# Kernel tuning notes

Measured on AMD Instinct MI355X. Metric: run time of the kernel, lower is better.

Reference implementation:

```python
import jax, jax.numpy as jnp
import numpy as np

EPS = 1e-5
C = 256
K = 3
K2 = K * K


def conv2d(x, w, b=None, groups=1):
    out = jax.lax.conv_general_dilated(
        x, w, (1, 1), 'VALID',
        dimension_numbers=('NCHW', 'OIHW', 'NCHW'),
        feature_group_count=groups)
    if b is not None:
        out = out + b[None, :, None, None]
    return out


def _bilinear_one(img, py, px):
    # img: [C,H,W]; py,px: [K2,ho,wo] float sampling coords (zero outside)
    _, H, W = img.shape
    y0 = jnp.floor(py)
    x0 = jnp.floor(px)
    dy = py - y0
    dx = px - x0
    y0i = y0.astype(jnp.int32)
    x0i = x0.astype(jnp.int32)

    def gather(yi, xi):
        valid = ((yi >= 0) & (yi < H) & (xi >= 0) & (xi < W)).astype(img.dtype)
        yc = jnp.clip(yi, 0, H - 1)
        xc = jnp.clip(xi, 0, W - 1)
        return img[:, yc, xc] * valid[None]  # [C,K2,ho,wo]

    w00 = (1 - dy) * (1 - dx)
    w01 = (1 - dy) * dx
    w10 = dy * (1 - dx)
    w11 = dy * dx
    return (gather(y0i, x0i) * w00[None] + gather(y0i, x0i + 1) * w01[None]
            + gather(y0i + 1, x0i) * w10[None] + gather(y0i + 1, x0i + 1) * w11[None])


def deform_conv(x, off_w, off_b, w, b):
    # ModulatedDeformConvPack: 3x3, stride=1, pad=0, dil=1, deformable_groups=1
    B, Cin, H, W = x.shape
    ho, wo = H - 2, W - 2
    om = conv2d(x, off_w, off_b)  # [B, 3*K2, ho, wo]
    o1, o2, m = om[:, :K2], om[:, K2:2 * K2], om[:, 2 * K2:]
    offset = jnp.concatenate([o1, o2], axis=1)  # [B, 2*K2, ho, wo]
    off_y = offset[:, 0::2]  # kernel reads y at channel 2k
    off_x = offset[:, 1::2]  # and x at channel 2k+1
    mask = jax.nn.sigmoid(m)  # [B,K2,ho,wo]
    ky, kx = jnp.meshgrid(jnp.arange(K), jnp.arange(K), indexing='ij')
    base_y = (ky.reshape(K2, 1, 1) + jnp.arange(ho).reshape(1, ho, 1)).astype(x.dtype)
    base_x = (kx.reshape(K2, 1, 1) + jnp.arange(wo).reshape(1, 1, wo)).astype(x.dtype)
    py = base_y[None] + off_y
    px = base_x[None] + off_x
    samples = jax.vmap(_bilinear_one)(x, py, px)  # [B,C,K2,ho,wo]
    samples = samples * mask[:, None]
    out = jnp.einsum('bckhw,ock->bohw', samples, w.reshape(w.shape[0], Cin, K2))
    return out + b[None, :, None, None]


def bn(x, g, b_, m, v):
    scale = g / jnp.sqrt(v + EPS)
    return (x - m[None, :, None, None]) * scale[None, :, None, None] + b_[None, :, None, None]


def xcorr(inst, exam):
    # batch-as-groups depthwise cross-correlation
    B = exam.shape[0]
    w = exam.reshape(B * C, 1, 18, 18)
    x = inst.reshape(1, B * C, 30, 30)
    out = jax.lax.conv_general_dilated(
        x, w, (1, 1), 'VALID',
        dimension_numbers=('NCHW', 'OIHW', 'NCHW'),
        feature_group_count=B * C)
    return out.reshape(B, C, 13, 13)


def _forward(examplar, instance, off_w, off_b, dcn_w, dcn_b,
             bn1_g, bn1_b, bn1_m, bn1_v,
             fus_w, fus_b, bn2_g, bn2_b, bn2_m, bn2_v,
             cls_w, cls_b, box_w, box_b):
    def head(x, i):  # deform conv + BN (eval)
        y = deform_conv(x, off_w[i], off_b[i], dcn_w[i], dcn_b[i])
        return bn(y, bn1_g[i], bn1_b[i], bn1_m[i], bn1_v[i])

    exam_cls = head(examplar, 0)
    inst_cls = head(instance, 1)
    exam_reg = head(examplar, 2)
    inst_reg = head(instance, 3)

    xc_cls = xcorr(inst_cls, exam_cls)
    xc_reg = xcorr(inst_reg, exam_reg)

    def fuse(x, i):  # 1x1 conv + BN + ReLU
        y = jnp.einsum('bchw,oc->bohw', x, fus_w[i]) + fus_b[i][None, :, None, None]
        return jax.nn.relu(bn(y, bn2_g[i], bn2_b[i], bn2_m[i], bn2_v[i]))

    f_cls = fuse(xc_cls, 0)
    f_reg = fuse(xc_reg, 1)

    cls_pred = jnp.einsum('bchw,oc->bohw', f_cls, cls_w) + cls_b[None, :, None, None]
    box_pred = jnp.einsum('bchw,oc->bohw', f_reg, box_w) + box_b[None, :, None, None]
    return cls_pred, box_pred


def setup_inputs() -> dict:
    key = jax.random.key(0)
    ks = jax.random.split(key, 24)
    B = 16
    d = {
        'examplar': jax.random.normal(ks[0], (B, C, 20, 20), jnp.float32),
        'instance': jax.random.normal(ks[1], (B, C, 32, 32), jnp.float32),
        # 4 deform heads: 0=exam_cls, 1=inst_cls, 2=exam_reg, 3=inst_reg
        'off_w': jax.random.normal(ks[2], (4, 3 * K2, C, K, K), jnp.float32) * 0.01,
        'off_b': jax.random.normal(ks[3], (4, 3 * K2), jnp.float32) * 0.01,
        'dcn_w': jax.random.normal(ks[4], (4, C, C, K, K), jnp.float32) * 0.05,
        'dcn_b': jax.random.normal(ks[5], (4, C), jnp.float32) * 0.05,
        'bn1_g': jax.random.uniform(ks[6], (4, C), jnp.float32) + 0.5,
        'bn1_b': jax.random.normal(ks[7], (4, C), jnp.float32) * 0.1,
        'bn1_m': jax.random.normal(ks[8], (4, C), jnp.float32) * 0.1,
        'bn1_v': jax.random.uniform(ks[9], (4, C), jnp.float32) + 0.5,
        # 2 fusion modules: 0=cls, 1=reg
        'fus_w': jax.random.normal(ks[10], (2, C, C), jnp.float32) * 0.05,
        'fus_b': jax.random.normal(ks[11], (2, C), jnp.float32) * 0.05,
        'bn2_g': jax.random.uniform(ks[12], (2, C), jnp.float32) + 0.5,
        'bn2_b': jax.random.normal(ks[13], (2, C), jnp.float32) * 0.1,
        'bn2_m': jax.random.normal(ks[14], (2, C), jnp.float32) * 0.1,
        'bn2_v': jax.random.uniform(ks[15], (2, C), jnp.float32) + 0.5,
        'cls_w': jax.random.normal(ks[16], (4, C), jnp.float32) * 0.05,
        'cls_b': jax.random.normal(ks[17], (4,), jnp.float32) * 0.05,
        'box_w': jax.random.normal(ks[18], (16, C), jnp.float32) * 0.05,
        'box_b': jax.random.normal(ks[19], (16,), jnp.float32) * 0.05,
    }
    return d


def reference(examplar, instance, off_w, off_b, dcn_w, dcn_b,
              bn1_g, bn1_b, bn1_m, bn1_v,
              fus_w, fus_b, bn2_g, bn2_b, bn2_m, bn2_v,
              cls_w, cls_b, box_w, box_b):
    return _forward(examplar, instance, off_w, off_b, dcn_w, dcn_b,
                    bn1_g, bn1_b, bn1_m, bn1_v,
                    fus_w, fus_b, bn2_g, bn2_b, bn2_m, bn2_v,
                    cls_w, cls_b, box_w, box_b)
```

## Files before the change

### kernel.cpp

```cpp
#include <hip/hip_runtime.h>
#include <math.h>

#define EPSBN 1e-5f

typedef _Float16 f16x8 __attribute__((ext_vector_type(8)));
typedef _Float16 f16x2 __attribute__((ext_vector_type(2)));
typedef float    f32x4 __attribute__((ext_vector_type(4)));

__device__ __forceinline__ f16x8 splat8(float v) {
  _Float16 h = (_Float16)v;
  return (f16x8){h, h, h, h, h, h, h, h};
}

static constexpr size_t XF_EX = 0;
static constexpr size_t XF_IN = 819200;
static constexpr size_t WPK   = 2916352;
static constexpr size_t OWPK  = 4096000;
static constexpr size_t FWT   = 4243456;
static constexpr size_t OM0   = 4374528;
static constexpr size_t OM1   = 4514496;
static constexpr size_t OM2   = 4903296;
static constexpr size_t OM3   = 5043264;
static constexpr size_t HOUT0 = 5432064;
static constexpr size_t HOUT1 = 6759168;
static constexpr size_t HOUT2 = 10445568;
static constexpr size_t HOUT3 = 11772672;
static constexpr size_t XCB   = 15459072;

__global__ __launch_bounds__(256) void k_transpose(const float* __restrict__ in,
                                                   _Float16* __restrict__ out,
                                                   int H, int W) {
  int y = blockIdx.x, b = blockIdx.y;
  __shared__ float tile[32][257];
  int t = threadIdx.x;
  int x = t & 31, cb = t >> 5;
  for (int c0 = 0; c0 < 256; c0 += 8) {
    int c = c0 + cb;
    if (x < W) tile[x][c] = in[(((size_t)b * 256 + c) * H + y) * W + x];
  }
  __syncthreads();
  for (int x2 = 0; x2 < W; ++x2)
    out[((((size_t)b * H + y) * W + x2) << 8) + t] = (_Float16)tile[x2][t];
}

__global__ __launch_bounds__(256) void k_wpack(const float* __restrict__ w,
                                               _Float16* __restrict__ wp) {
  int idx = blockIdx.x * 256 + threadIdx.x;
  if (idx >= 4 * 9 * 8 * 16 * 64 * 8) return;
  int e  = idx & 7;
  int l  = (idx >> 3) & 63;
  int ot = (idx >> 9) & 15;
  int cs = (idx >> 13) & 7;
  int ht = idx >> 16;
  int tap = ht % 9, h = ht / 9;
  int o = ot * 16 + (l & 15);
  int c = cs * 32 + 8 * (l >> 4) + e;
  wp[idx] = (_Float16)w[((size_t)((h * 256 + o) * 256 + c)) * 9 + tap];
}

__global__ __launch_bounds__(256) void k_owpack(const float* __restrict__ w,
                                                _Float16* __restrict__ wp) {
  int idx = blockIdx.x * 256 + threadIdx.x;
  if (idx >= 4 * 9 * 8 * 2 * 64 * 8) return;
  int e  = idx & 7;
  int l  = (idx >> 3) & 63;
  int ot = (idx >> 9) & 1;
  int cs = (idx >> 10) & 7;
  int ht = idx >> 13;
  int tap = ht % 9, h = ht / 9;
  int o = ot * 16 + (l & 15);
  int c = cs * 32 + 8 * (l >> 4) + e;
  wp[idx] = (o < 27) ? (_Float16)w[((size_t)((h * 27 + o) * 256 + c)) * 9 + tap]
                     : (_Float16)0.f;
}

__global__ __launch_bounds__(256) void k_fwt(const float* __restrict__ w,
                                             float* __restrict__ wt) {
  int idx = blockIdx.x * 256 + threadIdx.x;
  int o = idx & 255, c = (idx >> 8) & 255, i = idx >> 16;
  wt[idx] = w[(i << 16) + (o << 8) + c];
}

__global__ __launch_bounds__(256) void k_offdirect(const _Float16* __restrict__ xh_ex,
                                                   const _Float16* __restrict__ xh_in,
                                                   const _Float16* __restrict__ owpk,
                                                   const float* __restrict__ off_b,
                                                   float* __restrict__ ws) {
  const int h = blockIdx.z, b = blockIdx.y;
  const int HH[4] = {20, 32, 20, 32};
  const size_t OMO[4] = {OM0, OM1, OM2, OM3};
  const int H = HH[h], W = H, ho = H - 2, wo = W - 2, P = ho * wo;
  const int nblk = (P + 63) >> 6;
  if (blockIdx.x >= nblk) return;
  const int p0 = blockIdx.x << 6;
  const _Float16* xh = ((h & 1) ? xh_in : xh_ex) + (((size_t)b * H * W) << 8);

  const int t = threadIdx.x, lane = t & 63, wave = t >> 6;
  int p = min(p0 + wave * 16 + (lane & 15), P - 1);
  int i = p / wo, j = p - i * wo;
  const _Float16* xrow = xh + ((i * W + j) << 8) + 8 * (lane >> 4);

  f32x4 acc0 = {0.f, 0.f, 0.f, 0.f}, acc1 = {0.f, 0.f, 0.f, 0.f};
  for (int tap = 0; tap < 9; ++tap) {
    int ky = tap / 3, kx = tap - ky * 3;
    const _Float16* xt = xrow + ((ky * W + kx) << 8);
    const _Float16* ab0 = owpk + ((size_t)(h * 72 + tap * 8) * 2) * 512 + lane * 8;
    #pragma unroll
    for (int cs = 0; cs < 8; ++cs) {
      f16x8 bf = *(const f16x8*)(xt + cs * 32);
      f16x8 a0 = *(const f16x8*)(ab0 + (size_t)cs * 1024);
      f16x8 a1 = *(const f16x8*)(ab0 + (size_t)cs * 1024 + 512);
      acc0 = __builtin_amdgcn_mfma_f32_16x16x32_f16(a0, bf, acc0, 0, 0, 0);
      acc1 = __builtin_amdgcn_mfma_f32_16x16x32_f16(a1, bf, acc1, 0, 0, 0);
    }
  }
  float* om = ws + OMO[h] + (size_t)b * 27 * P;
  p = p0 + wave * 16 + (lane & 15);
  if (p < P) {
    #pragma unroll
    for (int r = 0; r < 4; ++r) {
      int o = 4 * (lane >> 4) + r;
      if (o < 27) om[o * P + p] = acc0[r] + off_b[h * 27 + o];
      int o2 = o + 16;
      if (o2 < 27) om[o2 * P + p] = acc1[r] + off_b[h * 27 + o2];
    }
  }
}

__global__ __launch_bounds__(256) void k_dgemm(const _Float16* __restrict__ xh_ex,
                                               const _Float16* __restrict__ xh_in,
                                               const _Float16* __restrict__ wpk,
                                               float* __restrict__ ws,
                                               const float* __restrict__ dcn_b,
                                               const float* __restrict__ g1,
                                               const float* __restrict__ b1,
                                               const float* __restrict__ m1,
                                               const float* __restrict__ v1) {
  const int h = blockIdx.z;
  const int HH4[4] = {20, 32, 20, 32};
  const size_t OMO[4] = {OM0, OM1, OM2, OM3};
  const size_t HOO[4] = {HOUT0, HOUT1, HOUT2, HOUT3};
  const int H = HH4[h], W = H, ho = H - 2, wo = W - 2, P = ho * wo;
  const int nblk = (P + 63) >> 6;
  if (blockIdx.x >= nblk) return;
  const int b = blockIdx.y;
  const int p0 = blockIdx.x << 6;
  const _Float16* xh = (h & 1) ? xh_in : xh_ex;
  const float* om = ws + OMO[h] + (size_t)b * 27 * P;
  float* outp = ws + HOO[h] + (size_t)b * 256 * P;

  __shared__ float4 swt4[576];
  __shared__ int4   sad4[576];
  __shared__ __align__(16) _Float16 S[64 * 256];

  const int t = threadIdx.x, lane = t & 63, wave = t >> 6;

  for (int e = t; e < 576; e += 256) {
    int pl = e / 9, k = e - pl * 9;
    float w4[4] = {0.f, 0.f, 0.f, 0.f};
    int a4[4] = {0, 0, 0, 0};
    int p = p0 + pl;
    if (p < P) {
      int i = p / wo, j = p - i * wo;
      float oy = om[(2 * k) * P + p];
      float ox = om[(2 * k + 1) * P + p];
      float mm = om[(18 + k) * P + p];
      float msk = 1.f / (1.f + __expf(-mm));
      int ky = k / 3, kx = k - ky * 3;
      float py = (float)(ky + i) + oy;
      float px = (float)(kx + j) + ox;
      float fy = floorf(py), fx = floorf(px);
      int y0 = (int)fy, x0 = (int)fx;
      float dy = py - fy, dx = px - fx;
      #pragma unroll
      for (int q = 0; q < 4; ++q) {
        int yy = y0 + (q >> 1), xx = x0 + (q & 1);
        bool vld = (yy >= 0) && (yy < H) && (xx < W) && (xx >= 0);
        int yc = min(max(yy, 0), H - 1), xc = min(max(xx, 0), W - 1);
        float wq = ((q >> 1) ? dy : 1.f - dy) * ((q & 1) ? dx : 1.f - dx);
        w4[q] = vld ? wq * msk : 0.f;
        a4[q] = ((blockIdx.y * H + yc) * W + xc) << 8;
      }
    }
    swt4[e] = make_float4(w4[0], w4[1], w4[2], w4[3]);
    sad4[e] = make_int4(a4[0], a4[1], a4[2], a4[3]);
  }

  f32x4 acc[4][4];
  #pragma unroll
  for (int a = 0; a < 4; ++a)
    #pragma unroll
    for (int n = 0; n < 4; ++n) acc[a][n] = (f32x4){0.f, 0.f, 0.f, 0.f};

  __syncthreads();

  const int o8 = t & 31;
  for (int tap = 0; tap < 9; ++tap) {
    #pragma unroll
    for (int it = 0; it < 8; ++it) {
      int pl = it * 8 + (t >> 5);
      float4 w4 = swt4[pl * 9 + tap];
      int4   a4 = sad4[pl * 9 + tap];
      const _Float16* xb = xh + o8 * 8;
      f16x8 x0 = *(const f16x8*)(xb + a4.x);
      f16x8 x1 = *(const f16x8*)(xb + a4.y);
      f16x8 x2 = *(const f16x8*)(xb + a4.z);
      f16x8 x3 = *(const f16x8*)(xb + a4.w);
      f16x8 s = x0 * splat8(w4.x) + x1 * splat8(w4.y) + x2 * splat8(w4.z) + x3 * splat8(w4.w);
      *(f16x8*)((char*)S + pl * 512 + ((o8 * 16) ^ ((pl & 7) << 4))) = s;
    }
    __syncthreads();
    #pragma unroll
    for (int cs = 0; cs < 8; ++cs) {
      int ksg = tap * 8 + cs;
      const _Float16* ab = wpk + ((size_t)(h * 72 + ksg) * 16 + wave * 4) * 512 + lane * 8;
      f16x8 A0 = *(const f16x8*)(ab);
      f16x8 A1 = *(const f16x8*)(ab + 512);
      f16x8 A2 = *(const f16x8*)(ab + 1024);
      f16x8 A3 = *(const f16x8*)(ab + 1536);
      f16x8 B[4];
      #pragma unroll
      for (int n = 0; n < 4; ++n) {
        int prow = n * 16 + (lane & 15);
        B[n] = *(const f16x8*)((char*)S + prow * 512 +
                               ((cs * 64 + ((lane >> 4) << 4)) ^ ((prow & 7) << 4)));
      }
      #pragma unroll
      for (int n = 0; n < 4; ++n) {
        acc[0][n] = __builtin_amdgcn_mfma_f32_16x16x32_f16(A0, B[n], acc[0][n], 0, 0, 0);
        acc[1][n] = __builtin_amdgcn_mfma_f32_16x16x32_f16(A1, B[n], acc[1][n], 0, 0, 0);
        acc[2][n] = __builtin_amdgcn_mfma_f32_16x16x32_f16(A2, B[n], acc[2][n], 0, 0, 0);
        acc[3][n] = __builtin_amdgcn_mfma_f32_16x16x32_f16(A3, B[n], acc[3][n], 0, 0, 0);
      }
    }
    __syncthreads();
  }

  #pragma unroll
  for (int a = 0; a < 4; ++a) {
    int obase = (wave * 4 + a) * 16 + 4 * (lane >> 4);
    #pragma unroll
    for (int r = 0; r < 4; ++r) {
      int o = obase + r;
      float al = g1[h * 256 + o] * rsqrtf(v1[h * 256 + o] + EPSBN);
      float be = (dcn_b[h * 256 + o] - m1[h * 256 + o]) * al + b1[h * 256 + o];
      #pragma unroll
      for (int n = 0; n < 4; ++n) {
        int p = p0 + n * 16 + (lane & 15);
        if (p < P) outp[(size_t)o * P + p] = fmaf(acc[a][n][r], al, be);
      }
    }
  }
}

__global__ __launch_bounds__(256) void k_xcorr3(float* __restrict__ ws) {
  const int br = blockIdx.y;
  const int bc0 = blockIdx.x << 4;
  const float* exg = ws + (br ? HOUT2 : HOUT0) + (size_t)bc0 * 324;
  const float* ing = ws + (br ? HOUT3 : HOUT1) + (size_t)bc0 * 900;
  __shared__ __align__(16) _Float16 exl[16 * 324];
  __shared__ __align__(16) _Float16 inl[16 * 960];
  const int t = threadIdx.x;
  for (int idx = t; idx < 16 * 324; idx += 256)
    exl[idx] = (_Float16)exg[idx];
  for (int idx = t; idx < 16 * 960; idx += 256) {
    int c = idx & 31;
    int rr = idx >> 5;
    inl[idx] = (c < 30) ? (_Float16)ing[rr * 30 + c] : (_Float16)0.f;
  }
  __syncthreads();
  const int lane = t & 63, wave = t >> 6;
  const int sub = lane / 13;
  const int i = lane - sub * 13;
  const bool active = sub < 4;
  const int bcl = wave * 4 + (active ? sub : 0);
  float acc[13];
  #pragma unroll
  for (int j = 0; j < 13; ++j) acc[j] = 0.f;
  const _Float16* inb = inl + bcl * 960;
  const _Float16* exb = exl + bcl * 324;
  for (int u = 0; u < 18; ++u) {
    float a[30];
    const _Float16* rp = inb + (i + u) * 32;
    #pragma unroll
    for (int x = 0; x < 15; ++x) {
      f16x2 pr = *(const f16x2*)(rp + 2 * x);
      a[2 * x] = (float)pr[0]; a[2 * x + 1] = (float)pr[1];
    }
    float e[18];
    const _Float16* ep = exb + u * 18;
    #pragma unroll
    for (int x = 0; x < 9; ++x) {
      f16x2 pr = *(const f16x2*)(ep + 2 * x);
      e[2 * x] = (float)pr[0]; e[2 * x + 1] = (float)pr[1];
    }
    #pragma unroll
    for (int v = 0; v < 18; ++v)
      #pragma unroll
      for (int j = 0; j < 13; ++j)
        acc[j] = fmaf(a[v + j], e[v], acc[j]);
  }
  if (active) {
    float* o = ws + XCB + ((size_t)(br * 4096 + bc0 + bcl)) * 169 + i * 13;
    #pragma unroll
    for (int j = 0; j < 13; ++j) o[j] = acc[j];
  }
}

__global__ __launch_bounds__(256) void k_fuse2(float* __restrict__ ws,
                                               const float* __restrict__ fus_b,
                                               const float* __restrict__ g2,
                                               const float* __restrict__ b2,
                                               const float* __restrict__ m2,
                                               const float* __restrict__ v2,
                                               const float* __restrict__ cls_w,
                                               const float* __restrict__ cls_b,
                                               const float* __restrict__ box_w,
                                               const float* __restrict__ box_b,
                                               float* __restrict__ out) {
  const int ij0 = blockIdx.x * 13;
  const int b = blockIdx.y;
  const int br = blockIdx.z;
  const int n_out = br ? 16 : 4;
  const float* ow = br ? box_w : cls_w;
  const float* ob = br ? box_b : cls_b;
  float* outp = out + (br ? (size_t)10816 : 0);

  __shared__ float xv[256 * 13];
  __shared__ float fv[13 * 257];
  const int t = threadIdx.x;
  const float* src = ws + XCB + ((size_t)br * 4096 + b * 256) * 169;
  for (int idx = t; idx < 256 * 13; idx += 256) {
    int c = idx / 13, j = idx - c * 13;
    xv[idx] = src[(size_t)c * 169 + ij0 + j];
  }
  __syncthreads();

  const float* fwt = ws + FWT + ((size_t)br << 16) + t;
  float acc[13];
  #pragma unroll
  for (int j = 0; j < 13; ++j) acc[j] = 0.f;
  for (int c = 0; c < 256; ++c) {
    float wv = fwt[c << 8];
    #pragma unroll
    for (int j = 0; j < 13; ++j)
      acc[j] = fmaf(wv, xv[c * 13 + j], acc[j]);
  }
  float s2 = g2[br * 256 + t] * rsqrtf(v2[br * 256 + t] + EPSBN);
  float fb = fus_b[br * 256 + t], mm = m2[br * 256 + t], bb = b2[br * 256 + t];
  #pragma unroll
  for (int j = 0; j < 13; ++j)
    fv[j * 257 + t] = fmaxf((acc[j] + fb - mm) * s2 + bb, 0.f);
  __syncthreads();

  const int g = t >> 4, l16 = t & 15;
  for (int wi = g; wi < 13 * n_out; wi += 16) {
    int j = wi / n_out, po = wi - j * n_out;
    float part = 0.f;
    #pragma unroll
    for (int q = 0; q < 16; ++q)
      part = fmaf(ow[(po << 8) + l16 + (q << 4)], fv[j * 257 + l16 + (q << 4)], part);
    #pragma unroll
    for (int off = 8; off; off >>= 1) part += __shfl_xor(part, off);
    if (l16 == 0)
      outp[((size_t)b * n_out + po) * 169 + ij0 + j] = part + ob[po];
  }
}

extern "C" void kernel_launch(void* const* d_in, const int* in_sizes, int n_in,
                              void* d_out, int out_size, void* d_ws, size_t ws_size,
                              hipStream_t stream) {
  const float* ex    = (const float*)d_in[0];
  const float* inst  = (const float*)d_in[1];
  const float* off_w = (const float*)d_in[2];
  const float* off_b = (const float*)d_in[3];
  const float* dcn_w = (const float*)d_in[4];
  const float* dcn_b = (const float*)d_in[5];
  const float* bn1_g = (const float*)d_in[6];
  const float* bn1_b = (const float*)d_in[7];
  const float* bn1_m = (const float*)d_in[8];
  const float* bn1_v = (const float*)d_in[9];
  const float* fus_w = (const float*)d_in[10];
  const float* fus_b = (const float*)d_in[11];
  const float* bn2_g = (const float*)d_in[12];
  const float* bn2_b = (const float*)d_in[13];
  const float* bn2_m = (const float*)d_in[14];
  const float* bn2_v = (const float*)d_in[15];
  const float* cls_w = (const float*)d_in[16];
  const float* cls_b = (const float*)d_in[17];
  const float* box_w = (const float*)d_in[18];
  const float* box_b = (const float*)d_in[19];
  float* out = (float*)d_out;
  float* ws  = (float*)d_ws;

  _Float16* xh_ex = (_Float16*)(ws + XF_EX);
  _Float16* xh_in = (_Float16*)(ws + XF_IN);
  _Float16* wpk   = (_Float16*)(ws + WPK);
  _Float16* owpk  = (_Float16*)(ws + OWPK);

  k_transpose<<<dim3(20, 16), 256, 0, stream>>>(ex,   xh_ex, 20, 20);
  k_transpose<<<dim3(32, 16), 256, 0, stream>>>(inst, xh_in, 32, 32);
  k_wpack <<<9216, 256, 0, stream>>>(dcn_w, wpk);
  k_owpack<<<1152, 256, 0, stream>>>(off_w, owpk);
  k_fwt   <<<512, 256, 0, stream>>>(fus_w, ws + FWT);
  k_offdirect<<<dim3(15, 16, 4), 256, 0, stream>>>(xh_ex, xh_in, owpk, off_b, ws);
  k_dgemm<<<dim3(15, 16, 4), 256, 0, stream>>>(xh_ex, xh_in, wpk, ws,
                                               dcn_b, bn1_g, bn1_b, bn1_m, bn1_v);
  k_xcorr3<<<dim3(256, 2), 256, 0, stream>>>(ws);
  k_fuse2<<<dim3(13, 16, 2), 256, 0, stream>>>(ws, fus_b, bn2_g, bn2_b, bn2_m, bn2_v,
                                               cls_w, cls_b, box_w, box_b, out);
}
```

Baseline: 341.4 us.

## Prefetch deformable gathers and batch weight loads to overlap memory with MFMA

In the deformable GEMM kernel, bilinear corner gathers are now loaded into registers ahead of use. The next tap's first half is prefetched before the MFMA phase, and the second half is loaded while the first half is combined, so global-load latency overlaps LDS writes and matrix math. The MFMA loop now processes two channel slices per iteration with all A and B operands loaded up front. The offset-conv kernel likewise batches its loads before issuing its MFMAs. These changes raise register pressure (16 f16x8 gather registers plus larger operand sets), which may reduce occupancy.

```diff
diff --git a/kernel.cpp b/kernel.cpp
--- a/kernel.cpp
+++ b/kernel.cpp
@@ -81,11 +81,11 @@
   wt[idx] = w[(i << 16) + (o << 8) + c];
 }
 
-__global__ __launch_bounds__(256) void k_offdirect(const _Float16* __restrict__ xh_ex,
-                                                   const _Float16* __restrict__ xh_in,
-                                                   const _Float16* __restrict__ owpk,
-                                                   const float* __restrict__ off_b,
-                                                   float* __restrict__ ws) {
+__global__ __launch_bounds__(256) void k_offbatch(const _Float16* __restrict__ xh_ex,
+                                                  const _Float16* __restrict__ xh_in,
+                                                  const _Float16* __restrict__ owpk,
+                                                  const float* __restrict__ off_b,
+                                                  float* __restrict__ ws) {
   const int h = blockIdx.z, b = blockIdx.y;
   const int HH[4] = {20, 32, 20, 32};
   const size_t OMO[4] = {OM0, OM1, OM2, OM3};
@@ -105,13 +105,17 @@
     int ky = tap / 3, kx = tap - ky * 3;
     const _Float16* xt = xrow + ((ky * W + kx) << 8);
     const _Float16* ab0 = owpk + ((size_t)(h * 72 + tap * 8) * 2) * 512 + lane * 8;
+    f16x8 bf[8], a0[8], a1[8];
     #pragma unroll
     for (int cs = 0; cs < 8; ++cs) {
-      f16x8 bf = *(const f16x8*)(xt + cs * 32);
-      f16x8 a0 = *(const f16x8*)(ab0 + (size_t)cs * 1024);
-      f16x8 a1 = *(const f16x8*)(ab0 + (size_t)cs * 1024 + 512);
-      acc0 = __builtin_amdgcn_mfma_f32_16x16x32_f16(a0, bf, acc0, 0, 0, 0);
-      acc1 = __builtin_amdgcn_mfma_f32_16x16x32_f16(a1, bf, acc1, 0, 0, 0);
+      bf[cs] = *(const f16x8*)(xt + cs * 32);
+      a0[cs] = *(const f16x8*)(ab0 + (size_t)cs * 1024);
+      a1[cs] = *(const f16x8*)(ab0 + (size_t)cs * 1024 + 512);
+    }
+    #pragma unroll
+    for (int cs = 0; cs < 8; ++cs) {
+      acc0 = __builtin_amdgcn_mfma_f32_16x16x32_f16(a0[cs], bf[cs], acc0, 0, 0, 0);
+      acc1 = __builtin_amdgcn_mfma_f32_16x16x32_f16(a1[cs], bf[cs], acc1, 0, 0, 0);
     }
   }
   float* om = ws + OMO[h] + (size_t)b * 27 * P;
@@ -175,7 +179,7 @@
       #pragma unroll
       for (int q = 0; q < 4; ++q) {
         int yy = y0 + (q >> 1), xx = x0 + (q & 1);
-        bool vld = (yy >= 0) && (yy < H) && (xx < W) && (xx >= 0);
+        bool vld = (yy >= 0) && (yy < H) && (xx >= 0) && (xx < W);
         int yc = min(max(yy, 0), H - 1), xc = min(max(xx, 0), W - 1);
         float wq = ((q >> 1) ? dy : 1.f - dy) * ((q & 1) ? dx : 1.f - dx);
         w4[q] = vld ? wq * msk : 0.f;
@@ -195,42 +199,95 @@
   __syncthreads();
 
   const int o8 = t & 31;
+  const int plq = t >> 5;
+  const _Float16* xb = xh + o8 * 8;
+
+  f16x8 gx[16];
+  #pragma unroll
+  for (int it = 0; it < 4; ++it) {
+    int e = (it * 8 + plq) * 9;
+    int4 a4 = sad4[e];
+    gx[it * 4 + 0] = *(const f16x8*)(xb + a4.x);
+    gx[it * 4 + 1] = *(const f16x8*)(xb + a4.y);
+    gx[it * 4 + 2] = *(const f16x8*)(xb + a4.z);
+    gx[it * 4 + 3] = *(const f16x8*)(xb + a4.w);
+  }
+
   for (int tap = 0; tap < 9; ++tap) {
     #pragma unroll
-    for (int it = 0; it < 8; ++it) {
-      int pl = it * 8 + (t >> 5);
+    for (int it = 0; it < 4; ++it) {
+      int pl = it * 8 + plq;
       float4 w4 = swt4[pl * 9 + tap];
-      int4   a4 = sad4[pl * 9 + tap];
-      const _Float16* xb = xh + o8 * 8;
-      f16x8 x0 = *(const f16x8*)(xb + a4.x);
-      f16x8 x1 = *(const f16x8*)(xb + a4.y);
-      f16x8 x2 = *(const f16x8*)(xb + a4.z);
-      f16x8 x3 = *(const f16x8*)(xb + a4.w);
-      f16x8 s = x0 * splat8(w4.x) + x1 * splat8(w4.y) + x2 * splat8(w4.z) + x3 * splat8(w4.w);
+      f16x8 s = gx[it * 4 + 0] * splat8(w4.x) + gx[it * 4 + 1] * splat8(w4.y)
+              + gx[it * 4 + 2] * splat8(w4.z) + gx[it * 4 + 3] * splat8(w4.w);
       *(f16x8*)((char*)S + pl * 512 + ((o8 * 16) ^ ((pl & 7) << 4))) = s;
     }
+    #pragma unroll
+    for (int it = 0; it < 4; ++it) {
+      int e = ((it + 4) * 8 + plq) * 9 + tap;
+      int4 a4 = sad4[e];
+      gx[it * 4 + 0] = *(const f16x8*)(xb + a4.x);
+      gx[it * 4 + 1] = *(const f16x8*)(xb + a4.y);
+      gx[it * 4 + 2] = *(const f16x8*)(xb + a4.z);
+      gx[it * 4 + 3] = *(const f16x8*)(xb + a4.w);
+    }
+    #pragma unroll
+    for (int it = 0; it < 4; ++it) {
+      int pl = (it + 4) * 8 + plq;
+      float4 w4 = swt4[pl * 9 + tap];
+      f16x8 s = gx[it * 4 + 0] * splat8(w4.x) + gx[it * 4 + 1] * splat8(w4.y)
+              + gx[it * 4 + 2] * splat8(w4.z) + gx[it * 4 + 3] * splat8(w4.w);
+      *(f16x8*)((char*)S + pl * 512 + ((o8 * 16) ^ ((pl & 7) << 4))) = s;
+    }
     __syncthreads();
-    #pragma unroll
-    for (int cs = 0; cs < 8; ++cs) {
-      int ksg = tap * 8 + cs;
-      const _Float16* ab = wpk + ((size_t)(h * 72 + ksg) * 16 + wave * 4) * 512 + lane * 8;
-      f16x8 A0 = *(const f16x8*)(ab);
-      f16x8 A1 = *(const f16x8*)(ab + 512);
-      f16x8 A2 = *(const f16x8*)(ab + 1024);
-      f16x8 A3 = *(const f16x8*)(ab + 1536);
-      f16x8 B[4];
+    if (tap < 8) {
+      #pragma unroll
+      for (int it = 0; it < 4; ++it) {
+        int e = (it * 8 + plq) * 9 + tap + 1;
+        int4 a4 = sad4[e];
+        gx[it * 4 + 0] = *(const f16x8*)(xb + a4.x);
+        gx[it * 4 + 1] = *(const f16x8*)(xb + a4.y);
+        gx[it * 4 + 2] = *(const f16x8*)(xb + a4.z);
+        gx[it * 4 + 3] = *(const f16x8*)(xb + a4.w);
+      }
+    }
+    #pragma unroll
+    for (int csp = 0; csp < 4; ++csp) {
+      int cs0 = 2 * csp;
+      const _Float16* ab0 = wpk + ((size_t)(h * 72 + tap * 8 + cs0) * 16 + wave * 4) * 512 + lane * 8;
+      const _Float16* ab1 = ab0 + 16 * 512;
+      f16x8 A[8];
+      A[0] = *(const f16x8*)(ab0);
+      A[1] = *(const f16x8*)(ab0 + 512);
+      A[2] = *(const f16x8*)(ab0 + 1024);
+      A[3] = *(const f16x8*)(ab0 + 1536);
+      A[4] = *(const f16x8*)(ab1);
+      A[5] = *(const f16x8*)(ab1 + 512);
+      A[6] = *(const f16x8*)(ab1 + 1024);
+      A[7] = *(const f16x8*)(ab1 + 1536);
+      f16x8 B0[4], B1[4];
       #pragma unroll
       for (int n = 0; n < 4; ++n) {
         int prow = n * 16 + (lane & 15);
-        B[n] = *(const f16x8*)((char*)S + prow * 512 +
-                               ((cs * 64 + ((lane >> 4) << 4)) ^ ((prow & 7) << 4)));
+        int swz = (prow & 7) << 4;
+        B0[n] = *(const f16x8*)((char*)S + prow * 512 +
+                                ((cs0 * 64 + ((lane >> 4) << 4)) ^ swz));
+        B1[n] = *(const f16x8*)((char*)S + prow * 512 +
+                                (((cs0 + 1) * 64 + ((lane >> 4) << 4)) ^ swz));
       }
       #pragma unroll
       for (int n = 0; n < 4; ++n) {
-        acc[0][n] = __builtin_amdgcn_mfma_f32_16x16x32_f16(A0, B[n], acc[0][n], 0, 0, 0);
-        acc[1][n] = __builtin_amdgcn_mfma_f32_16x16x32_f16(A1, B[n], acc[1][n], 0, 0, 0);
-        acc[2][n] = __builtin_amdgcn_mfma_f32_16x16x32_f16(A2, B[n], acc[2][n], 0, 0, 0);
-        acc[3][n] = __builtin_amdgcn_mfma_f32_16x16x32_f16(A3, B[n], acc[3][n], 0, 0, 0);
+        acc[0][n] = __builtin_amdgcn_mfma_f32_16x16x32_f16(A[0], B0[n], acc[0][n], 0, 0, 0);
+        acc[1][n] = __builtin_amdgcn_mfma_f32_16x16x32_f16(A[1], B0[n], acc[1][n], 0, 0, 0);
+        acc[2][n] = __builtin_amdgcn_mfma_f32_16x16x32_f16(A[2], B0[n], acc[2][n], 0, 0, 0);
+        acc[3][n] = __builtin_amdgcn_mfma_f32_16x16x32_f16(A[3], B0[n], acc[3][n], 0, 0, 0);
+      }
+      #pragma unroll
+      for (int n = 0; n < 4; ++n) {
+        acc[0][n] = __builtin_amdgcn_mfma_f32_16x16x32_f16(A[4], B1[n], acc[0][n], 0, 0, 0);
+        acc[1][n] = __builtin_amdgcn_mfma_f32_16x16x32_f16(A[5], B1[n], acc[1][n], 0, 0, 0);
+        acc[2][n] = __builtin_amdgcn_mfma_f32_16x16x32_f16(A[6], B1[n], acc[2][n], 0, 0, 0);
+        acc[3][n] = __builtin_amdgcn_mfma_f32_16x16x32_f16(A[7], B1[n], acc[3][n], 0, 0, 0);
       }
     }
     __syncthreads();
@@ -403,7 +460,7 @@
   k_wpack <<<9216, 256, 0, stream>>>(dcn_w, wpk);
   k_owpack<<<1152, 256, 0, stream>>>(off_w, owpk);
   k_fwt   <<<512, 256, 0, stream>>>(fus_w, ws + FWT);
-  k_offdirect<<<dim3(15, 16, 4), 256, 0, stream>>>(xh_ex, xh_in, owpk, off_b, ws);
+  k_offbatch<<<dim3(15, 16, 4), 256, 0, stream>>>(xh_ex, xh_in, owpk, off_b, ws);
   k_dgemm<<<dim3(15, 16, 4), 256, 0, stream>>>(xh_ex, xh_in, wpk, ws,
                                                dcn_b, bn1_g, bn1_b, bn1_m, bn1_v);
   k_xcorr3<<<dim3(256, 2), 256, 0, stream>>>(ws);
```

Measured after the change: 364.1 us. 6.7% more time.
